# Kernel tuning notes

Measured on AMD Instinct MI355X. Metric: run time of the kernel, lower is better.

## Reference

```python
import math
import jax, jax.numpy as jnp
import numpy as np
from jax import lax

B, C, O, K, WDIM, H, W = 8, 512, 512, 3, 512, 64, 64
CONV_SCALE = 1.0 / math.sqrt(C * K * K)
MOD_SCALE = 1.0 / math.sqrt(WDIM)


def setup_inputs() -> dict:
    key = jax.random.key(0)
    k1, k2, k3, k4 = jax.random.split(key, 4)
    return {
        "x": jax.random.normal(k1, (B, C, H, W), dtype=jnp.float32),
        "w": jax.random.normal(k2, (B, WDIM), dtype=jnp.float32),
        "base_weight": jax.random.normal(k3, (1, O, C, K, K), dtype=jnp.float32),
        "mod_weight": jax.random.normal(k4, (C, WDIM), dtype=jnp.float32),
        "mod_bias": jnp.zeros((C,), dtype=jnp.float32),
    }


def reference(x, w, base_weight, mod_weight, mod_bias):
    # EqualLinear modulation: s in (B, C), then +1
    s = w @ (mod_weight * MOD_SCALE).T + mod_bias + 1.0  # (B, C)
    # Per-sample modulated weights: (B, O, C, K, K)
    weight = CONV_SCALE * base_weight * s[:, None, :, None, None]
    # Demodulation
    d = lax.rsqrt(jnp.sum(weight * weight, axis=(2, 3, 4), keepdims=True))
    weight = weight * d
    pad = K // 2

    def conv_one(xi, wi):
        # xi: (C, H, W), wi: (O, C, K, K)
        return lax.conv_general_dilated(
            xi[None], wi, window_strides=(1, 1),
            padding=[(pad, pad), (pad, pad)],
            dimension_numbers=("NCHW", "OIHW", "NCHW"),
        )[0]

    return jax.vmap(conv_one)(x, weight)  # (B, O, H, W)
```

## Files before the change

### kernel.cpp

```cpp
#include <hip/hip_runtime.h>
#include <stdint.h>


#define MOD_SCALE  0.044194173824159216f
#define CONV_SCALE 0.014731391274719739f

typedef __attribute__((ext_vector_type(4))) float f32x4;
typedef __attribute__((ext_vector_type(8))) short bf16x8;

__device__ inline unsigned short f2bf(float f) {
  uint32_t u = __float_as_uint(f);
  uint32_t r = (u + 0x7fffu + ((u >> 16) & 1u)) >> 16;
  return (unsigned short)r;
}

__device__ inline void gload_lds16(const void* g, void* l) {
  __builtin_amdgcn_global_load_lds(
      (const __attribute__((address_space(1))) void*)g,
      (__attribute__((address_space(3))) void*)l, 16, 0, 0);
}

__global__ __launch_bounds__(256) void k_style(const float* __restrict__ w,
                                               const float* __restrict__ modw,
                                               const float* __restrict__ modb,
                                               float* __restrict__ s_out) {
  __shared__ float red[256];
  const int t = threadIdx.x;
  const int cb = blockIdx.x, b = blockIdx.y;
  const int cl = t >> 2, q = t & 3;
  const int c = (cb << 6) + cl;
  const float4* wd = (const float4*)(w + (b << 9) + (q << 7));
  const float4* md = (const float4*)(modw + ((size_t)c << 9) + (q << 7));
  float acc = 0.f;
#pragma unroll
  for (int i = 0; i < 32; ++i) {
    float4 a = wd[i], m = md[i];
    acc += a.x * m.x + a.y * m.y + a.z * m.z + a.w * m.w;
  }
  red[t] = acc;
  __syncthreads();
  if (t < 64) {
    float v = red[t * 4] + red[t * 4 + 1] + red[t * 4 + 2] + red[t * 4 + 3];
    int cc = (cb << 6) + t;
    s_out[(b << 9) + cc] = v * MOD_SCALE + modb[cc] + 1.0f;
  }
}

__global__ __launch_bounds__(256) void k_fw(const float* __restrict__ bw,
                                            const float* __restrict__ s,
                                            unsigned short* __restrict__ wm) {
  __shared__ float lw[4608];
  __shared__ float ls[4096];
  __shared__ float red[32];
  __shared__ float sc8[8];
  const int tid = threadIdx.x;
  const int o = blockIdx.x;
  {
    const float4* src = (const float4*)(bw + (size_t)o * 4608);
    float4* dst = (float4*)lw;
#pragma unroll
    for (int i = 0; i < 4; ++i) dst[tid + (i << 8)] = src[tid + (i << 8)];
    if (tid < 128) dst[tid + 1024] = src[tid + 1024];
  }
  {
    const float4* src = (const float4*)s;
    float4* dst = (float4*)ls;
#pragma unroll
    for (int i = 0; i < 4; ++i) dst[tid + (i << 8)] = src[tid + (i << 8)];
  }
  __syncthreads();
  const int c0 = tid << 1;
  const int base = c0 * 9;
  float wq0 = 0.f, wq1 = 0.f;
#pragma unroll
  for (int j = 0; j < 9; ++j) {
    float a = lw[base + j];     wq0 += a * a;
    float b2 = lw[base + 9 + j]; wq1 += b2 * b2;
  }
  const int lane = tid & 63, wv = tid >> 6;
#pragma unroll
  for (int b = 0; b < 8; ++b) {
    float s0 = ls[(b << 9) + c0], s1 = ls[(b << 9) + c0 + 1];
    float v = wq0 * s0 * s0 + wq1 * s1 * s1;
#pragma unroll
    for (int off = 32; off > 0; off >>= 1) v += __shfl_down(v, off, 64);
    if (lane == 0) red[(b << 2) + wv] = v;
  }
  __syncthreads();
  if (tid < 8) {
    float a = red[tid << 2] + red[(tid << 2) + 1] + red[(tid << 2) + 2] + red[(tid << 2) + 3];
    sc8[tid] = rsqrtf(a * (1.0f / 4608.0f)) * CONV_SCALE;
  }
  __syncthreads();
#pragma unroll 1
  for (int b = 0; b < 8; ++b) {
    const float dsc = sc8[b];
    const float s0 = ls[(b << 9) + c0] * dsc;
    const float s1 = ls[(b << 9) + c0 + 1] * dsc;
    uint32_t* dst = (uint32_t*)(wm + (size_t)((b << 9) + o) * 4608);
#pragma unroll
    for (int j = 0; j < 9; ++j) {
      float v0 = lw[base + j] * s0;
      float v1 = lw[base + 9 + j] * s1;
      dst[(j << 8) + tid] = (uint32_t)f2bf(v0) | ((uint32_t)f2bf(v1) << 16);
    }
  }
}

__global__ __launch_bounds__(256) void k_border(unsigned short* __restrict__ xp) {
  int p = blockIdx.x, b = blockIdx.y;
  int py, px;
  if (p < 66)       { py = 0;       px = p; }
  else if (p < 132) { py = 65;      px = p - 66; }
  else if (p < 196) { py = p - 131; px = 0; }
  else              { py = p - 195; px = 65; }
  uint32_t* dst = (uint32_t*)(xp + ((size_t)b * 4356 + py * 66 + px) * 512);
  dst[threadIdx.x] = 0u;
}

__global__ __launch_bounds__(256) void k_xpose(const float* __restrict__ x,
                                               unsigned short* __restrict__ xp) {
  __shared__ unsigned short tile[64 * 65];
  const int b = blockIdx.z, c0 = blockIdx.y << 6, p0 = blockIdx.x << 6;
  const int tid = threadIdx.x;
  {
    const int pi = tid & 63, ci0 = tid >> 6;
    const float* src = x + (size_t)((b << 9) + c0 + ci0) * 4096 + p0 + pi;
#pragma unroll
    for (int it = 0; it < 16; ++it)
      tile[(ci0 + (it << 2)) * 65 + pi] = f2bf(src[(size_t)(it << 2) * 4096]);
  }
  __syncthreads();
  {
    const int co = tid & 63, po0 = tid >> 6;
#pragma unroll
    for (int it = 0; it < 16; ++it) {
      int p = po0 + (it << 2);
      int gp = p0 + p;
      int py = (gp >> 6) + 1, px = (gp & 63) + 1;
      xp[((size_t)b * 4356 + py * 66 + px) * 512 + c0 + co] = tile[co * 65 + p];
    }
  }
}

__global__ __launch_bounds__(256, 4) void k_conv(const unsigned short* __restrict__ wmodT,
                                                 const unsigned short* __restrict__ xpad,
                                                 float* __restrict__ out) {
  __shared__ alignas(16) unsigned short As[8192];
  __shared__ alignas(16) unsigned short Bs[8192];
  const int tid = threadIdx.x;
  const int b  = blockIdx.z;
  const int m0 = blockIdx.y << 7;
  const int n0 = blockIdx.x << 7;
  const int y0 = n0 >> 6;

  const int srow = tid >> 3;
  const int schk = ((tid & 7) - (srow & 7)) & 7;
  const int scol = schk << 3;

  const unsigned short* Ag = wmodT + (size_t)((b << 9) + m0 + srow) * 4608 + scol;
  const size_t bx = (size_t)b * (66 * 66 * 512);

  const int lane = tid & 63;
  const int wv   = tid >> 6;
  const int moff = (wv >> 1) << 6;
  const int noff = (wv & 1) << 6;
  const int lm   = lane & 15;
  const int g4   = lane >> 4;

  const unsigned short* ardA[2];
  const unsigned short* ardB[2];
#pragma unroll
  for (int h = 0; h < 2; ++h) {
    ardA[h] = As + (moff + lm) * 64 + ((((h << 2) + g4) + moff + lm) & 7) * 8;
    ardB[h] = Bs + (noff + lm) * 64 + ((((h << 2) + g4) + noff + lm) & 7) * 8;
  }

  f32x4 acc[4][4];
#pragma unroll
  for (int i = 0; i < 4; ++i)
#pragma unroll
    for (int j = 0; j < 4; ++j) acc[i][j] = (f32x4){0.f, 0.f, 0.f, 0.f};

#pragma unroll 1
  for (int tap = 0; tap < 9; ++tap) {
    const int ky = (tap * 11) >> 5;
    const int kx = tap - ky * 3;
    const unsigned short* Bt[4];
#pragma unroll
    for (int g = 0; g < 4; ++g) {
      const int n = (g << 5) + srow;
      Bt[g] = xpad + bx +
              (size_t)((y0 + ky + (n >> 6)) * 66 + kx + (n & 63)) * 512 + scol;
    }
#pragma unroll 1
    for (int kb = 0; kb < 8; ++kb) {
#pragma unroll
      for (int g = 0; g < 4; ++g)
        gload_lds16(Ag + g * (32 * 4608), As + (((g << 8) + tid) << 3));
#pragma unroll
      for (int g = 0; g < 4; ++g)
        gload_lds16(Bt[g] + (kb << 6), Bs + (((g << 8) + tid) << 3));
      Ag += 64;
      __syncthreads();
#pragma unroll
      for (int h = 0; h < 2; ++h) {
        bf16x8 af[4], bf[4];
#pragma unroll
        for (int i = 0; i < 4; ++i) af[i] = *(const bf16x8*)(ardA[h] + (i << 10));
#pragma unroll
        for (int j = 0; j < 4; ++j) bf[j] = *(const bf16x8*)(ardB[h] + (j << 10));
#pragma unroll
        for (int i = 0; i < 4; ++i)
#pragma unroll
          for (int j = 0; j < 4; ++j)
            acc[i][j] = __builtin_amdgcn_mfma_f32_16x16x32_bf16(af[i], bf[j], acc[i][j], 0, 0, 0);
      }
      __syncthreads();
    }
  }

  float* op = out + (size_t)((b << 9) + m0 + moff) * 4096 + n0 + noff;
#pragma unroll
  for (int i = 0; i < 4; ++i) {
#pragma unroll
    for (int r = 0; r < 4; ++r) {
      const int m = i * 16 + (g4 << 2) + r;
#pragma unroll
      for (int j = 0; j < 4; ++j)
        op[(size_t)m * 4096 + (j << 4) + lm] = acc[i][j][r];
    }
  }
}

extern "C" void kernel_launch(void* const* d_in, const int* in_sizes, int n_in,
                              void* d_out, int out_size, void* d_ws, size_t ws_size,
                              hipStream_t stream) {
  const float* x    = (const float*)d_in[0];
  const float* w    = (const float*)d_in[1];
  const float* bw   = (const float*)d_in[2];
  const float* modw = (const float*)d_in[3];
  const float* modb = (const float*)d_in[4];
  float* out = (float*)d_out;
  char* ws = (char*)d_ws;

  float* s_buf = (float*)(ws);
  unsigned short* wmod = (unsigned short*)(ws + 16384);
  unsigned short* xpad = (unsigned short*)(ws + 37765120);

  (void)in_sizes; (void)n_in; (void)out_size; (void)ws_size;

  k_style <<<dim3(8, 8), 256, 0, stream>>>(w, modw, modb, s_buf);
  k_fw    <<<512, 256, 0, stream>>>(bw, s_buf, wmod);
  k_border<<<dim3(260, 8), 256, 0, stream>>>(xpad);
  k_xpose <<<dim3(64, 8, 8), 256, 0, stream>>>(x, xpad);
  k_conv  <<<dim3(32, 4, 8), 256, 0, stream>>>(wmod, xpad, out);
}
```

Measured before the change: 301.2 us.

## Reuse padded input row across kx taps and fuse prep kernels

```diff
diff --git a/kernel.cpp b/kernel.cpp
--- a/kernel.cpp
+++ b/kernel.cpp
@@ -20,29 +20,69 @@
       (__attribute__((address_space(3))) void*)l, 16, 0, 0);
 }
 
-__global__ __launch_bounds__(256) void k_style(const float* __restrict__ w,
-                                               const float* __restrict__ modw,
-                                               const float* __restrict__ modb,
-                                               float* __restrict__ s_out) {
-  __shared__ float red[256];
-  const int t = threadIdx.x;
-  const int cb = blockIdx.x, b = blockIdx.y;
-  const int cl = t >> 2, q = t & 3;
-  const int c = (cb << 6) + cl;
-  const float4* wd = (const float4*)(w + (b << 9) + (q << 7));
-  const float4* md = (const float4*)(modw + ((size_t)c << 9) + (q << 7));
-  float acc = 0.f;
-#pragma unroll
-  for (int i = 0; i < 32; ++i) {
-    float4 a = wd[i], m = md[i];
-    acc += a.x * m.x + a.y * m.y + a.z * m.z + a.w * m.w;
-  }
-  red[t] = acc;
-  __syncthreads();
-  if (t < 64) {
-    float v = red[t * 4] + red[t * 4 + 1] + red[t * 4 + 2] + red[t * 4 + 3];
-    int cc = (cb << 6) + t;
-    s_out[(b << 9) + cc] = v * MOD_SCALE + modb[cc] + 1.0f;
+__global__ __launch_bounds__(256) void k_prep(const float* __restrict__ x,
+                                              const float* __restrict__ w,
+                                              const float* __restrict__ modw,
+                                              const float* __restrict__ modb,
+                                              unsigned short* __restrict__ xp,
+                                              float* __restrict__ s_out) {
+  __shared__ unsigned short smem[64 * 65];
+  const int blk = blockIdx.x;
+  const int tid = threadIdx.x;
+  if (blk < 4096) {
+    const int b = blk >> 9, r = blk & 511;
+    const int c0 = ((r >> 6) << 6), p0 = ((r & 63) << 6);
+    {
+      const int pi = tid & 63, ci0 = tid >> 6;
+      const float* src = x + (size_t)((b << 9) + c0 + ci0) * 4096 + p0 + pi;
+#pragma unroll
+      for (int it = 0; it < 16; ++it)
+        smem[(ci0 + (it << 2)) * 65 + pi] = f2bf(src[(size_t)(it << 2) * 4096]);
+    }
+    __syncthreads();
+    {
+      const int cq = tid & 31, pq = tid >> 5;
+#pragma unroll
+      for (int it = 0; it < 8; ++it) {
+        const int p = pq + (it << 3);
+        const int gp = p0 + p;
+        const int py = (gp >> 6) + 1, px = (gp & 63) + 1;
+        uint32_t v = (uint32_t)smem[(cq << 1) * 65 + p] |
+                     ((uint32_t)smem[((cq << 1) + 1) * 65 + p] << 16);
+        ((uint32_t*)(xp + ((size_t)b * 4356 + py * 66 + px) * 512 + c0))[cq] = v;
+      }
+    }
+  } else if (blk < 6176) {
+    const int q = blk - 4096;
+    const int b = q / 260, p = q - b * 260;
+    int py, px;
+    if (p < 66)       { py = 0;       px = p; }
+    else if (p < 132) { py = 65;      px = p - 66; }
+    else if (p < 196) { py = p - 131; px = 0; }
+    else              { py = p - 195; px = 65; }
+    uint32_t* dst = (uint32_t*)(xp + ((size_t)b * 4356 + py * 66 + px) * 512);
+    dst[tid] = 0u;
+  } else {
+    float* red = (float*)smem;
+    const int sb = blk - 6176;
+    const int cb = sb & 7, b = sb >> 3;
+    const int cl = tid >> 2, qq = tid & 3;
+    const int c = (cb << 6) + cl;
+    const float4* wd = (const float4*)(w + (b << 9) + (qq << 7));
+    const float4* md = (const float4*)(modw + ((size_t)c << 9) + (qq << 7));
+    float acc = 0.f;
+#pragma unroll
+    for (int i = 0; i < 32; ++i) {
+      float4 a = wd[i], m = md[i];
+      acc += a.x * m.x + a.y * m.y + a.z * m.z + a.w * m.w;
+    }
+    red[tid] = acc;
+    __syncthreads();
+    if (tid < 64) {
+      float v = red[tid * 4] + red[tid * 4 + 1] + red[tid * 4 + 2] + red[tid * 4 + 3];
+      int cc = (cb << 6) + tid;
+      s_out[(b << 9) + cc] = v * MOD_SCALE + modb[cc] + 1.0f;
+    }
   }
 }
 
@@ -74,7 +114,7 @@
   float wq0 = 0.f, wq1 = 0.f;
 #pragma unroll
   for (int j = 0; j < 9; ++j) {
-    float a = lw[base + j];     wq0 += a * a;
+    float a = lw[base + j];      wq0 += a * a;
     float b2 = lw[base + 9 + j]; wq1 += b2 * b2;
   }
   const int lane = tid & 63, wv = tid >> 6;
@@ -107,47 +147,11 @@
   }
 }
 
-__global__ __launch_bounds__(256) void k_border(unsigned short* __restrict__ xp) {
-  int p = blockIdx.x, b = blockIdx.y;
-  int py, px;
-  if (p < 66)       { py = 0;       px = p; }
-  else if (p < 132) { py = 65;      px = p - 66; }
-  else if (p < 196) { py = p - 131; px = 0; }
-  else              { py = p - 195; px = 65; }
-  uint32_t* dst = (uint32_t*)(xp + ((size_t)b * 4356 + py * 66 + px) * 512);
-  dst[threadIdx.x] = 0u;
-}
-
-__global__ __launch_bounds__(256) void k_xpose(const float* __restrict__ x,
-                                               unsigned short* __restrict__ xp) {
-  __shared__ unsigned short tile[64 * 65];
-  const int b = blockIdx.z, c0 = blockIdx.y << 6, p0 = blockIdx.x << 6;
-  const int tid = threadIdx.x;
-  {
-    const int pi = tid & 63, ci0 = tid >> 6;
-    const float* src = x + (size_t)((b << 9) + c0 + ci0) * 4096 + p0 + pi;
-#pragma unroll
-    for (int it = 0; it < 16; ++it)
-      tile[(ci0 + (it << 2)) * 65 + pi] = f2bf(src[(size_t)(it << 2) * 4096]);
-  }
-  __syncthreads();
-  {
-    const int co = tid & 63, po0 = tid >> 6;
-#pragma unroll
-    for (int it = 0; it < 16; ++it) {
-      int p = po0 + (it << 2);
-      int gp = p0 + p;
-      int py = (gp >> 6) + 1, px = (gp & 63) + 1;
-      xp[((size_t)b * 4356 + py * 66 + px) * 512 + c0 + co] = tile[co * 65 + p];
-    }
-  }
-}
-
-__global__ __launch_bounds__(256, 4) void k_conv(const unsigned short* __restrict__ wmodT,
+__global__ __launch_bounds__(256, 2) void k_conv(const unsigned short* __restrict__ wmodT,
                                                  const unsigned short* __restrict__ xpad,
                                                  float* __restrict__ out) {
-  __shared__ alignas(16) unsigned short As[8192];
-  __shared__ alignas(16) unsigned short Bs[8192];
+  __shared__ alignas(16) unsigned short As[3 * 8192];
+  __shared__ alignas(16) unsigned short Bs[8448];
   const int tid = threadIdx.x;
   const int b  = blockIdx.z;
   const int m0 = blockIdx.y << 7;
@@ -158,22 +162,28 @@
   const int schk = ((tid & 7) - (srow & 7)) & 7;
   const int scol = schk << 3;
 
-  const unsigned short* Ag = wmodT + (size_t)((b << 9) + m0 + srow) * 4608 + scol;
+  const unsigned short* A0 = wmodT + (size_t)((b << 9) + m0 + srow) * 4608 + scol;
   const size_t bx = (size_t)b * (66 * 66 * 512);
 
   const int lane = tid & 63;
   const int wv   = tid >> 6;
   const int moff = (wv >> 1) << 6;
   const int noff = (wv & 1) << 6;
+  const int noffp = noff ? 66 : 0;
   const int lm   = lane & 15;
   const int g4   = lane >> 4;
 
   const unsigned short* ardA[2];
-  const unsigned short* ardB[2];
-#pragma unroll
-  for (int h = 0; h < 2; ++h) {
+#pragma unroll
+  for (int h = 0; h < 2; ++h)
     ardA[h] = As + (moff + lm) * 64 + ((((h << 2) + g4) + moff + lm) & 7) * 8;
-    ardB[h] = Bs + (noff + lm) * 64 + ((((h << 2) + g4) + noff + lm) & 7) * 8;
+  const unsigned short* ardB[3][2];
+#pragma unroll
+  for (int kx = 0; kx < 3; ++kx) {
+    const int rb = noffp + lm + kx;
+#pragma unroll
+    for (int h = 0; h < 2; ++h)
+      ardB[kx][h] = Bs + rb * 64 + ((((h << 2) + g4) + rb) & 7) * 8;
   }
 
   f32x4 acc[4][4];
@@ -183,38 +193,41 @@
     for (int j = 0; j < 4; ++j) acc[i][j] = (f32x4){0.f, 0.f, 0.f, 0.f};
 
 #pragma unroll 1
-  for (int tap = 0; tap < 9; ++tap) {
-    const int ky = (tap * 11) >> 5;
-    const int kx = tap - ky * 3;
-    const unsigned short* Bt[4];
-#pragma unroll
-    for (int g = 0; g < 4; ++g) {
-      const int n = (g << 5) + srow;
-      Bt[g] = xpad + bx +
-              (size_t)((y0 + ky + (n >> 6)) * 66 + kx + (n & 63)) * 512 + scol;
-    }
+  for (int ky = 0; ky < 3; ++ky) {
+    const unsigned short* Bp0 = xpad + bx + (size_t)((y0 + ky) * 66 + srow) * 512 + scol;
 #pragma unroll 1
     for (int kb = 0; kb < 8; ++kb) {
+      const int kcol = kb << 6;
+#pragma unroll
+      for (int kx = 0; kx < 3; ++kx) {
+        const unsigned short* Ap = A0 + ((ky * 3 + kx) << 9) + kcol;
+#pragma unroll
+        for (int g = 0; g < 4; ++g)
+          gload_lds16(Ap + g * (32 * 4608), As + ((kx << 13) + (((g << 8) + tid) << 3)));
+      }
+      const unsigned short* Bp = Bp0 + kcol;
 #pragma unroll
       for (int g = 0; g < 4; ++g)
-        gload_lds16(Ag + g * (32 * 4608), As + (((g << 8) + tid) << 3));
-#pragma unroll
-      for (int g = 0; g < 4; ++g)
-        gload_lds16(Bt[g] + (kb << 6), Bs + (((g << 8) + tid) << 3));
-      Ag += 64;
+        gload_lds16(Bp + g * (32 * 512), Bs + (((g << 8) + tid) << 3));
+      if (tid < 32) gload_lds16(Bp + 128 * 512, Bs + 8192 + tid * 8);
       __syncthreads();
 #pragma unroll
-      for (int h = 0; h < 2; ++h) {
-        bf16x8 af[4], bf[4];
-#pragma unroll
-        for (int i = 0; i < 4; ++i) af[i] = *(const bf16x8*)(ardA[h] + (i << 10));
-#pragma unroll
-        for (int j = 0; j < 4; ++j) bf[j] = *(const bf16x8*)(ardB[h] + (j << 10));
-#pragma unroll
-        for (int i = 0; i < 4; ++i)
-#pragma unroll
-          for (int j = 0; j < 4; ++j)
-            acc[i][j] = __builtin_amdgcn_mfma_f32_16x16x32_bf16(af[i], bf[j], acc[i][j], 0, 0, 0);
+      for (int kx = 0; kx < 3; ++kx) {
+#pragma unroll
+        for (int h = 0; h < 2; ++h) {
+          bf16x8 af[4], bf[4];
+          const unsigned short* pa = ardA[h] + (kx << 13);
+          const unsigned short* pb = ardB[kx][h];
+#pragma unroll
+          for (int i = 0; i < 4; ++i) af[i] = *(const bf16x8*)(pa + (i << 10));
+#pragma unroll
+          for (int j = 0; j < 4; ++j) bf[j] = *(const bf16x8*)(pb + (j << 10));
+#pragma unroll
+          for (int i = 0; i < 4; ++i)
+#pragma unroll
+            for (int j = 0; j < 4; ++j)
+              acc[i][j] = __builtin_amdgcn_mfma_f32_16x16x32_bf16(af[i], bf[j], acc[i][j], 0, 0, 0);
+        }
       }
       __syncthreads();
     }
@@ -250,9 +263,7 @@
 
   (void)in_sizes; (void)n_in; (void)out_size; (void)ws_size;
 
-  k_style <<<dim3(8, 8), 256, 0, stream>>>(w, modw, modb, s_buf);
-  k_fw    <<<512, 256, 0, stream>>>(bw, s_buf, wmod);
-  k_border<<<dim3(260, 8), 256, 0, stream>>>(xpad);
-  k_xpose <<<dim3(64, 8, 8), 256, 0, stream>>>(x, xpad);
-  k_conv  <<<dim3(32, 4, 8), 256, 0, stream>>>(wmod, xpad, out);
-}
+  k_prep<<<6240, 256, 0, stream>>>(x, w, modw, modb, xpad, s_buf);
+  k_fw  <<<512, 256, 0, stream>>>(bw, s_buf, wmod);
+  k_conv<<<dim3(32, 4, 8), 256, 0, stream>>>(wmod, xpad, out);
+}
```

After: 265.6 us. 11.8% less time.
